# Optimization experiments

Hardware: AMD Instinct MI355X
Metric: run time of the kernel (lower is better)

Reference implementation:

```python
import jax, jax.numpy as jnp
import numpy as np

L = 6  # num_objects (greedy iterations)
BIG = 1e8  # penalty for already-used template ids (matches torch code)


def setup_inputs() -> dict:
    key = jax.random.key(0)
    k1, k2, k3, k4 = jax.random.split(key, 4)
    B, T, C, H, W = 16, 144, 1, 128, 128
    x = jax.random.uniform(k1, (B, C, H, W), jnp.float32)
    templates = jax.random.uniform(k2, (B, T, C, H, W), jnp.float32)
    masks = jax.random.uniform(k3, (B, T, 1, H, W), jnp.float32)
    background = jax.random.uniform(k4, (1, C, H, W), jnp.float32)
    return {"x": x, "templates": templates, "masks": masks, "background": background}


def _greedy_select(x, templates, masks, background):
    """Greedy template selection. Faithful to DecompModel._greedy_selection
    (use_empty is falsy by default -> empty template = 5*ones, empty mask = ones).
    Key identity used for efficiency: dead-leaves composition of the l
    already-selected objects is affine in whatever lies below them:
        recons = A + Mprod * below,
    where A accumulates painted objects and Mprod = prod(1 - mask_i).
    The new candidate at step l is painted BELOW the existing selection
    (it sits at the last index, and compose_templates paints last->first),
    so below = cand*cand_mask + bg*(1-cand_mask). Identical math, no
    O(B*T*l) recomposition per step."""
    B, T = templates.shape[0], templates.shape[1]
    H, W = templates.shape[-2], templates.shape[-1]
    empty_t = 5.0 * jnp.ones((B, 1) + templates.shape[2:], templates.dtype)
    empty_m = jnp.ones((B, 1) + masks.shape[2:], masks.dtype)
    temps = jnp.concatenate([empty_t, templates], axis=1)   # (B,T+1,C,H,W)
    ms = jnp.concatenate([empty_m, masks], axis=1)           # (B,T+1,1,H,W)
    bg = jnp.broadcast_to(background, (B,) + background.shape[1:])  # (B,C,H,W)

    A0 = jnp.zeros_like(bg)                                  # painted-so-far
    M0 = jnp.ones((B, 1, H, W), bg.dtype)                    # transmission
    used0 = jnp.zeros((B, T + 1), bool)
    bidx = jnp.arange(B)

    def step(carry, _):
        A, Mprod, used = carry
        below = temps * ms + bg[:, None] * (1.0 - ms)        # (B,T+1,C,H,W)
        recons = A[:, None] + Mprod[:, None] * below         # (B,T+1,C,H,W)
        errors = jnp.mean((x[:, None] - recons) ** 2, axis=(2, 3, 4))  # (B,T+1)
        errors = jnp.where(used, BIG, errors)
        ids = jnp.argmin(errors, axis=1)                     # (B,)
        hit = (jnp.arange(T + 1)[None, :] == ids[:, None]) & (ids[:, None] != 0)
        used = used | hit                                    # empty id=0 reusable
        sel_t = temps[bidx, ids]                             # (B,C,H,W)
        sel_m = ms[bidx, ids]                                # (B,1,H,W)
        A = A + Mprod * sel_t * sel_m
        Mprod = Mprod * (1.0 - sel_m)
        return (A, Mprod, used), ids

    (_, _, _), ids = jax.lax.scan(step, (A0, M0, used0), None, length=L)
    ids = ids.T                                              # (B,L)
    objects = temps[bidx[:, None], ids]                      # (B,L,C,H,W)
    omasks = ms[bidx[:, None], ids]                          # (B,L,1,H,W)
    return objects, omasks, ids


def _compose(objects, omasks, background):
    """Dead-leaves composition, painting from last object to first
    (first selected object ends up on top), as in compose_templates."""
    B, N = objects.shape[0], objects.shape[1]
    recons = jnp.broadcast_to(background, (B,) + background.shape[1:])
    for i in range(N):  # small fixed loop over L objects
        o = objects[:, N - 1 - i]
        m = omasks[:, N - 1 - i]
        recons = o * m + recons * (1.0 - m)
    return recons


def reference(x, templates, masks, background):
    objects, omasks, ids = _greedy_select(x, templates, masks, background)
    recons = _compose(objects, omasks, background)           # (B,C,H,W)
    return recons, objects, omasks, ids
```

## Files before the change

### kernel.cpp

```cpp
#include <hip/hip_runtime.h>
#include <math.h>

#define BB 16
#define TT 144
#define TP1 145
#define HW4 4096
#define HW8 2048
#define LL 6
#define BIGE 1e30
#define NB_STEP (BB * TP1)
#define CHUNK 290
#define EPSQ 7.62951e-6

typedef float          f4    __attribute__((ext_vector_type(4)));
typedef float          f8    __attribute__((ext_vector_type(8)));
typedef unsigned short u16x4 __attribute__((ext_vector_type(4)));
typedef unsigned short u16x8 __attribute__((ext_vector_type(8)));

static const size_t OFF_A     = 0;
static const size_t OFF_M     = 1u << 20;
static const size_t OFF_U     = 2u << 20;
static const size_t OFF_V     = 3u << 20;
static const size_t OFF_ERR32 = 4u << 20;
static const size_t OFF_ERR16 = (4u << 20) + 32768;
static const size_t OFF_D     = (4u << 20) + 65536;
static const size_t OFF_USED  = (4u << 20) + 81920;
static const size_t OFF_WQ    = (4u << 20) + 131072;
static const size_t WS_FULL   = OFF_WQ + 75497472ull;

__device__ __forceinline__ float hsum(f4 v) { return ((v.x + v.y) + v.z) + v.w; }
__device__ __forceinline__ float hsum8(f8 v) {
    return (((v.s0 + v.s1) + (v.s2 + v.s3)) + ((v.s4 + v.s5) + (v.s6 + v.s7)));
}

__device__ __forceinline__ double blk_reduce(double s) {
    for (int off = 32; off; off >>= 1) s += __shfl_down(s, off);
    __shared__ double smr[4];
    if ((threadIdx.x & 63) == 0) smr[threadIdx.x >> 6] = s;
    __syncthreads();
    return smr[0] + smr[1] + smr[2] + smr[3];
}

__device__ __forceinline__ void blk_reduce2(double& a, double& b) {
    for (int off = 32; off; off >>= 1) { a += __shfl_down(a, off); b += __shfl_down(b, off); }
    __shared__ double sa[4], sb[4];
    if ((threadIdx.x & 63) == 0) { sa[threadIdx.x >> 6] = a; sb[threadIdx.x >> 6] = b; }
    __syncthreads();
    a = sa[0] + sa[1] + sa[2] + sa[3];
    b = sb[0] + sb[1] + sb[2] + sb[3];
}

__global__ void k_build(const f4* __restrict__ temps, const f4* __restrict__ masks,
                        const f4* __restrict__ bg, const f4* __restrict__ x,
                        u16x4* __restrict__ wq, double* __restrict__ err32,
                        int* __restrict__ used) {
    const int t = blockIdx.x, b = blockIdx.y, tid = threadIdx.x;
    const f4* xb = x + (size_t)b * HW4;
    double s = 0.0;
    if (t == 0) {
        if (tid < TP1) used[b * TP1 + tid] = 0;
        for (int j = tid; j < HW4; j += 256)
            s += (double)(100.f - 10.f * hsum(xb[j]));
    } else {
        const size_t row = ((size_t)(b * TT + t - 1)) * HW4;
        for (int j = tid; j < HW4; j += 256) {
            f4 tv = __builtin_nontemporal_load(&temps[row + j]);
            f4 mv = __builtin_nontemporal_load(&masks[row + j]);
            f4 bv = bg[j], xv = xb[j];
            f4 w = tv * mv + bv * (1.f - mv);
            wq[row + j] = __builtin_convertvector(w * 65535.f + 0.5f, u16x4);
            s += (double)hsum(w * (w - 2.f * xv));
        }
    }
    double tot = blk_reduce(s);
    if (tid == 0) err32[b * TP1 + t] = tot;
}

__global__ void k_err16(const u16x8* __restrict__ wq,
                        const f4* __restrict__ u4, const f4* __restrict__ v4,
                        const int* __restrict__ used,
                        double* __restrict__ err16, double* __restrict__ D) {
    const int lin = blockIdx.x;
    const int wg  = (lin & 7) * CHUNK + (lin >> 3);
    const int b   = wg / TP1;
    const int t   = wg - b * TP1;
    const int tid = threadIdx.x;
    if (t != 0 && used[b * TP1 + t]) {
        if (tid == 0) err16[b * TP1 + t] = BIGE;
        return;
    }
    if (t == 0) {
        const f4* ub = u4 + (size_t)b * HW4;
        const f4* vb = v4 + (size_t)b * HW4;
        double s = 0.0, d = 0.0;
        for (int j = tid; j < HW4; j += 256) {
            f4 uu = ub[j], vv = vb[j];
            s += (double)(25.f * hsum(vv) - 10.f * hsum(uu));
            f4 au = {fabsf(uu.x), fabsf(uu.y), fabsf(uu.z), fabsf(uu.w)};
            d += (double)hsum(vv + au);
        }
        blk_reduce2(s, d);
        if (tid == 0) { err16[b * TP1] = s; D[b] = d; }
        return;
    }
    const f8* ub = (const f8*)(u4 + (size_t)b * HW4);
    const f8* vb = (const f8*)(v4 + (size_t)b * HW4);
    const u16x8* wb = wq + ((size_t)(b * TT + t - 1)) * HW8;
    double s = 0.0;
    for (int j = tid; j < HW8; j += 256) {
        f8 w = __builtin_convertvector(wb[j], f8) * (1.f / 65535.f);
        f8 uu = ub[j], vv = vb[j];
        s += (double)hsum8(w * (vv * w - 2.f * uu));
    }
    double tot = blk_reduce(s);
    if (tid == 0) err16[b * TP1 + t] = tot;
}

__global__ void k_refine(const f4* __restrict__ temps, const f4* __restrict__ masks,
                         const f4* __restrict__ bg,
                         const f4* __restrict__ u4, const f4* __restrict__ v4,
                         const double* __restrict__ err16, const double* __restrict__ D,
                         double* __restrict__ err32) {
    const int t = blockIdx.x, b = blockIdx.y, tid = threadIdx.x;
    double e = (tid < TP1) ? err16[b * TP1 + tid] : 1e300;
    double m = e;
    for (int off = 32; off; off >>= 1) {
        double o = __shfl_down(m, off);
        m = (o < m) ? o : m;
    }
    __shared__ double sm[4]; __shared__ double smin_s; __shared__ int scnt[4];
    if ((tid & 63) == 0) sm[tid >> 6] = m;
    __syncthreads();
    if (tid == 0) {
        double a = (sm[0] < sm[1]) ? sm[0] : sm[1];
        double c = (sm[2] < sm[3]) ? sm[2] : sm[3];
        smin_s = (a < c) ? a : c;
    }
    __syncthreads();
    const double thr = smin_s + (4.0 * EPSQ * D[b] + 0.05);
    int flag = (tid < TP1) && (e <= thr);
    unsigned long long bal = __ballot(flag);
    if ((tid & 63) == 0) scnt[tid >> 6] = __popcll(bal);
    __syncthreads();
    const int cnt = scnt[0] + scnt[1] + scnt[2] + scnt[3];
    const double mys = err16[b * TP1 + t];
    if (mys > thr) { if (tid == 0) err32[b * TP1 + t] = BIGE; return; }
    if (cnt == 1 || t == 0) {
        if (tid == 0) err32[b * TP1 + t] = mys;
        return;
    }
    const f4* ub = u4 + (size_t)b * HW4;
    const f4* vb = v4 + (size_t)b * HW4;
    const size_t row = ((size_t)(b * TT + t - 1)) * HW4;
    double s = 0.0;
    for (int j = tid; j < HW4; j += 256) {
        f4 tv = temps[row + j], mv = masks[row + j], bv = bg[j];
        f4 uu = ub[j], vv = vb[j];
        f4 w = tv * mv + bv * (1.f - mv);
        s += (double)hsum(w * (vv * w - 2.f * uu));
    }
    double tot = blk_reduce(s);
    if (tid == 0) err32[b * TP1 + t] = tot;
}

__global__ void k_err_f32(const f4* __restrict__ temps, const f4* __restrict__ masks,
                          const f4* __restrict__ bg,
                          const f4* __restrict__ u4, const f4* __restrict__ v4,
                          const int* __restrict__ used, double* __restrict__ err32) {
    const int t = blockIdx.x, b = blockIdx.y, tid = threadIdx.x;
    if (t != 0 && used[b * TP1 + t]) {
        if (tid == 0) err32[b * TP1 + t] = BIGE;
        return;
    }
    const f4* ub = u4 + (size_t)b * HW4;
    const f4* vb = v4 + (size_t)b * HW4;
    double s = 0.0;
    if (t == 0) {
        for (int j = tid; j < HW4; j += 256) {
            f4 uu = ub[j], vv = vb[j];
            s += (double)(25.f * hsum(vv) - 10.f * hsum(uu));
        }
    } else {
        const size_t row = ((size_t)(b * TT + t - 1)) * HW4;
        for (int j = tid; j < HW4; j += 256) {
            f4 tv = temps[row + j], mv = masks[row + j], bv = bg[j];
            f4 uu = ub[j], vv = vb[j];
            f4 w = tv * mv + bv * (1.f - mv);
            s += (double)hsum(w * (vv * w - 2.f * uu));
        }
    }
    double tot = blk_reduce(s);
    if (tid == 0) err32[b * TP1 + t] = tot;
}

template <bool FIRST, bool LAST>
__global__ void k_upd(const f4* __restrict__ temps, const f4* __restrict__ masks,
                      const f4* __restrict__ x, const f4* __restrict__ bg,
                      const double* __restrict__ err,
                      int* __restrict__ used, f4* __restrict__ A, f4* __restrict__ M,
                      f4* __restrict__ u, f4* __restrict__ v,
                      f4* __restrict__ out_obj, f4* __restrict__ out_msk,
                      f4* __restrict__ out_rec, float* __restrict__ out_ids, int l) {
    const int tid = threadIdx.x;
    const int gid = blockIdx.x * 256 + tid;
    const int b = gid >> 12;
    const int p = gid & (HW4 - 1);
    __shared__ int ssel;
    if (tid < 64) {
        double best = 1e301;
        int bi = TP1;
        for (int t = tid; t < TP1; t += 64) {
            double e = err[b * TP1 + t];
            if (e < best) { best = e; bi = t; }
        }
        for (int off = 32; off; off >>= 1) {
            double oe = __shfl_down(best, off);
            int    oi = __shfl_down(bi, off);
            if (oe < best || (oe == best && oi < bi)) { best = oe; bi = oi; }
        }
        if (tid == 0) ssel = bi;
    }
    __syncthreads();
    const int id = ssel;
    f4 st, sm;
    if (id == 0) {
        st = (f4){5.f, 5.f, 5.f, 5.f};
        sm = (f4){1.f, 1.f, 1.f, 1.f};
    } else {
        size_t base = ((size_t)(b * TT + id - 1)) * HW4 + p;
        st = temps[base];
        sm = masks[base];
    }
    f4 a, mp;
    if (FIRST) { a = (f4){0.f, 0.f, 0.f, 0.f}; mp = (f4){1.f, 1.f, 1.f, 1.f}; }
    else       { a = A[gid]; mp = M[gid]; }
    a = a + mp * st * sm;
    mp = mp * (1.f - sm);
    const size_t ob = ((size_t)(b * LL + l)) * HW4 + p;
    out_obj[ob] = st;
    out_msk[ob] = sm;
    if (LAST) {
        out_rec[gid] = a + mp * bg[p];
    } else {
        A[gid] = a; M[gid] = mp;
        f4 xv = x[gid];
        u[gid] = (xv - a) * mp;
        v[gid] = mp * mp;
    }
    if ((blockIdx.x & 15) == 0 && tid == 0) {
        if (id != 0) used[b * TP1 + id] = 1;
        out_ids[b * LL + l] = (float)id;
    }
}

__global__ void k_uv0(const f4* __restrict__ x, f4* __restrict__ u, f4* __restrict__ v,
                      int* __restrict__ used) {
    int gid = blockIdx.x * blockDim.x + threadIdx.x;
    if (gid < BB * TP1) used[gid] = 0;
    if (gid >= BB * HW4) return;
    u[gid] = x[gid];
    v[gid] = (f4){1.f, 1.f, 1.f, 1.f};
}

static inline void launch_upd(bool first, bool last,
                              const f4* temps, const f4* masks, const f4* x, const f4* bg,
                              const double* err, int* used, f4* A, f4* M,
                              f4* u, f4* v, f4* out_obj, f4* out_msk, f4* out_rec,
                              float* out_ids, int l, hipStream_t stream) {
    if (first)
        k_upd<true, false><<<256, 256, 0, stream>>>(temps, masks, x, bg, err, used, A, M, u, v, out_obj, out_msk, out_rec, out_ids, l);
    else if (last)
        k_upd<false, true><<<256, 256, 0, stream>>>(temps, masks, x, bg, err, used, A, M, u, v, out_obj, out_msk, out_rec, out_ids, l);
    else
        k_upd<false, false><<<256, 256, 0, stream>>>(temps, masks, x, bg, err, used, A, M, u, v, out_obj, out_msk, out_rec, out_ids, l);
}

extern "C" void kernel_launch(void* const* d_in, const int* in_sizes, int n_in,
                              void* d_out, int out_size, void* d_ws, size_t ws_size,
                              hipStream_t stream) {
    const f4* x     = (const f4*)d_in[0];
    const f4* temps = (const f4*)d_in[1];
    const f4* masks = (const f4*)d_in[2];
    const f4* bg    = (const f4*)d_in[3];

    float* out      = (float*)d_out;
    f4*    out_rec  = (f4*)out;
    f4*    out_obj  = (f4*)(out + 262144);
    f4*    out_msk  = (f4*)(out + 262144 + 1572864);
    float* out_ids  = out + 262144 + 2 * 1572864;

    char* ws = (char*)d_ws;
    f4*     A     = (f4*)(ws + OFF_A);
    f4*     M     = (f4*)(ws + OFF_M);
    f4*     u     = (f4*)(ws + OFF_U);
    f4*     v     = (f4*)(ws + OFF_V);
    double* err32 = (double*)(ws + OFF_ERR32);
    double* err16 = (double*)(ws + OFF_ERR16);
    double* D     = (double*)(ws + OFF_D);
    int*    used  = (int*)(ws + OFF_USED);
    u16x4*  wq    = (u16x4*)(ws + OFF_WQ);

    const bool full = (ws_size >= WS_FULL);

    if (full) {
        k_build<<<dim3(TP1, BB), 256, 0, stream>>>(temps, masks, bg, x, wq, err32, used);
        for (int l = 0; l < LL; ++l) {
            launch_upd(l == 0, l == LL - 1, temps, masks, x, bg, err32, used, A, M, u, v,
                       out_obj, out_msk, out_rec, out_ids, l, stream);
            if (l < LL - 1) {
                k_err16<<<NB_STEP, 256, 0, stream>>>((const u16x8*)wq, u, v, used, err16, D);
                k_refine<<<dim3(TP1, BB), 256, 0, stream>>>(temps, masks, bg, u, v, err16, D, err32);
            }
        }
    } else {
        k_uv0<<<(BB * HW4 + 255) / 256, 256, 0, stream>>>(x, u, v, used);
        for (int l = 0; l < LL; ++l) {
            k_err_f32<<<dim3(TP1, BB), 256, 0, stream>>>(temps, masks, bg, u, v, used, err32);
            launch_upd(l == 0, l == LL - 1, temps, masks, x, bg, err32, used, A, M, u, v,
                       out_obj, out_msk, out_rec, out_ids, l, stream);
        }
    }
}
```

Baseline: 257.3 us.

## Batch four templates per block and reformulate error as residual squared norm

Build and per-step error kernels now process four templates per block, so the per-batch u/v (now scaled-mask and residual) vectors are loaded once and reused across four template rows. The state is cut from four arrays (A, M, u, v) to two (scaled transmission and residual), and the error becomes a direct squared-difference sum instead of an expanded quadratic. Block indices are swizzled across XCD-sized groups, and the refine threshold is widened to allow for the new formulation's quantization error. This trades fewer resident blocks and a looser refine filter, which may send more candidates to the fp32 path, for less redundant memory traffic.

```diff
diff --git a/kernel.cpp b/kernel.cpp
--- a/kernel.cpp
+++ b/kernel.cpp
@@ -8,29 +8,37 @@
 #define HW8 2048
 #define LL 6
 #define BIGE 1e30
-#define NB_STEP (BB * TP1)
-#define CHUNK 290
 #define EPSQ 7.62951e-6
+#define RB 37
+#define NBLK (BB * RB)
+#define BCHUNK 74
+#define RCHUNK 290
 
 typedef float          f4    __attribute__((ext_vector_type(4)));
 typedef float          f8    __attribute__((ext_vector_type(8)));
 typedef unsigned short u16x4 __attribute__((ext_vector_type(4)));
 typedef unsigned short u16x8 __attribute__((ext_vector_type(8)));
 
-static const size_t OFF_A     = 0;
-static const size_t OFF_M     = 1u << 20;
-static const size_t OFF_U     = 2u << 20;
-static const size_t OFF_V     = 3u << 20;
-static const size_t OFF_ERR32 = 4u << 20;
-static const size_t OFF_ERR16 = (4u << 20) + 32768;
-static const size_t OFF_D     = (4u << 20) + 65536;
-static const size_t OFF_USED  = (4u << 20) + 81920;
-static const size_t OFF_WQ    = (4u << 20) + 131072;
-static const size_t WS_FULL   = OFF_WQ + 75497472ull;
+static const size_t OFF_MS   = 0;
+static const size_t OFF_R    = 1u << 20;
+static const size_t OFF_E32  = 2u << 20;
+static const size_t OFF_E16  = (2u << 20) + 32768;
+static const size_t OFF_D    = (2u << 20) + 65536;
+static const size_t OFF_USED = (2u << 20) + 81920;
+static const size_t OFF_WQ   = 3u << 20;
+static const size_t WS_FULL  = OFF_WQ + 75497472ull;
 
 __device__ __forceinline__ float hsum(f4 v) { return ((v.x + v.y) + v.z) + v.w; }
 __device__ __forceinline__ float hsum8(f8 v) {
     return (((v.s0 + v.s1) + (v.s2 + v.s3)) + ((v.s4 + v.s5) + (v.s6 + v.s7)));
+}
+__device__ __forceinline__ f8 fabs8(f8 v) {
+    f8 o;
+    o.s0 = __builtin_fabsf(v.s0); o.s1 = __builtin_fabsf(v.s1);
+    o.s2 = __builtin_fabsf(v.s2); o.s3 = __builtin_fabsf(v.s3);
+    o.s4 = __builtin_fabsf(v.s4); o.s5 = __builtin_fabsf(v.s5);
+    o.s6 = __builtin_fabsf(v.s6); o.s7 = __builtin_fabsf(v.s7);
+    return o;
 }
 
 __device__ __forceinline__ double blk_reduce(double s) {
@@ -50,78 +58,129 @@
     b = sb[0] + sb[1] + sb[2] + sb[3];
 }
 
+__device__ __forceinline__ void blk_reduce4(double s[4]) {
+    for (int off = 32; off; off >>= 1) {
+        s[0] += __shfl_down(s[0], off); s[1] += __shfl_down(s[1], off);
+        s[2] += __shfl_down(s[2], off); s[3] += __shfl_down(s[3], off);
+    }
+    __shared__ double sm4[4][4];
+    const int wv = threadIdx.x >> 6;
+    if ((threadIdx.x & 63) == 0) {
+        sm4[wv][0] = s[0]; sm4[wv][1] = s[1]; sm4[wv][2] = s[2]; sm4[wv][3] = s[3];
+    }
+    __syncthreads();
+    for (int k = 0; k < 4; ++k) s[k] = sm4[0][k] + sm4[1][k] + sm4[2][k] + sm4[3][k];
+}
+
 __global__ void k_build(const f4* __restrict__ temps, const f4* __restrict__ masks,
                         const f4* __restrict__ bg, const f4* __restrict__ x,
                         u16x4* __restrict__ wq, double* __restrict__ err32,
                         int* __restrict__ used) {
-    const int t = blockIdx.x, b = blockIdx.y, tid = threadIdx.x;
+    const int lin = blockIdx.x;
+    const int wg = (lin & 7) * BCHUNK + (lin >> 3);
+    const int b = wg / RB, rg = wg - b * RB;
+    const int tid = threadIdx.x;
     const f4* xb = x + (size_t)b * HW4;
-    double s = 0.0;
-    if (t == 0) {
+    if (rg == RB - 1) {
         if (tid < TP1) used[b * TP1 + tid] = 0;
-        for (int j = tid; j < HW4; j += 256)
-            s += (double)(100.f - 10.f * hsum(xb[j]));
-    } else {
-        const size_t row = ((size_t)(b * TT + t - 1)) * HW4;
+        double s = 0.0;
         for (int j = tid; j < HW4; j += 256) {
-            f4 tv = __builtin_nontemporal_load(&temps[row + j]);
-            f4 mv = __builtin_nontemporal_load(&masks[row + j]);
-            f4 bv = bg[j], xv = xb[j];
-            f4 w = tv * mv + bv * (1.f - mv);
-            wq[row + j] = __builtin_convertvector(w * 65535.f + 0.5f, u16x4);
-            s += (double)hsum(w * (w - 2.f * xv));
-        }
-    }
-    double tot = blk_reduce(s);
-    if (tid == 0) err32[b * TP1 + t] = tot;
-}
-
-__global__ void k_err16(const u16x8* __restrict__ wq,
-                        const f4* __restrict__ u4, const f4* __restrict__ v4,
-                        const int* __restrict__ used,
-                        double* __restrict__ err16, double* __restrict__ D) {
-    const int lin = blockIdx.x;
-    const int wg  = (lin & 7) * CHUNK + (lin >> 3);
-    const int b   = wg / TP1;
-    const int t   = wg - b * TP1;
-    const int tid = threadIdx.x;
-    if (t != 0 && used[b * TP1 + t]) {
-        if (tid == 0) err16[b * TP1 + t] = BIGE;
+            f4 d = 5.f - xb[j];
+            s += (double)hsum(d * d);
+        }
+        double tot = blk_reduce(s);
+        if (tid == 0) err32[b * TP1 + 0] = tot;
         return;
     }
-    if (t == 0) {
-        const f4* ub = u4 + (size_t)b * HW4;
-        const f4* vb = v4 + (size_t)b * HW4;
+    const int tbase = 1 + rg * 4;
+    const size_t r0 = ((size_t)(b * TT + tbase - 1)) * HW4;
+    const size_t r1 = r0 + HW4, r2 = r1 + HW4, r3 = r2 + HW4;
+    double s[4] = {0.0, 0.0, 0.0, 0.0};
+    #pragma unroll 2
+    for (int j = tid; j < HW4; j += 256) {
+        f4 bv = bg[j], xv = xb[j];
+        f4 tv0 = __builtin_nontemporal_load(&temps[r0 + j]);
+        f4 mv0 = __builtin_nontemporal_load(&masks[r0 + j]);
+        f4 w0 = tv0 * mv0 + bv * (1.f - mv0);
+        wq[r0 + j] = __builtin_convertvector(w0 * 65535.f + 0.5f, u16x4);
+        f4 d0 = w0 - xv; s[0] += (double)hsum(d0 * d0);
+        f4 tv1 = __builtin_nontemporal_load(&temps[r1 + j]);
+        f4 mv1 = __builtin_nontemporal_load(&masks[r1 + j]);
+        f4 w1 = tv1 * mv1 + bv * (1.f - mv1);
+        wq[r1 + j] = __builtin_convertvector(w1 * 65535.f + 0.5f, u16x4);
+        f4 d1 = w1 - xv; s[1] += (double)hsum(d1 * d1);
+        f4 tv2 = __builtin_nontemporal_load(&temps[r2 + j]);
+        f4 mv2 = __builtin_nontemporal_load(&masks[r2 + j]);
+        f4 w2 = tv2 * mv2 + bv * (1.f - mv2);
+        wq[r2 + j] = __builtin_convertvector(w2 * 65535.f + 0.5f, u16x4);
+        f4 d2 = w2 - xv; s[2] += (double)hsum(d2 * d2);
+        f4 tv3 = __builtin_nontemporal_load(&temps[r3 + j]);
+        f4 mv3 = __builtin_nontemporal_load(&masks[r3 + j]);
+        f4 w3 = tv3 * mv3 + bv * (1.f - mv3);
+        wq[r3 + j] = __builtin_convertvector(w3 * 65535.f + 0.5f, u16x4);
+        f4 d3 = w3 - xv; s[3] += (double)hsum(d3 * d3);
+    }
+    blk_reduce4(s);
+    if (tid == 0)
+        for (int k = 0; k < 4; ++k) err32[b * TP1 + tbase + k] = s[k];
+}
+
+__global__ void k_errs(const u16x8* __restrict__ wq,
+                       const f8* __restrict__ Ms, const f8* __restrict__ R,
+                       const int* __restrict__ used,
+                       double* __restrict__ err16, double* __restrict__ Dd) {
+    const int lin = blockIdx.x;
+    const int wg = (lin & 7) * BCHUNK + (lin >> 3);
+    const int b = wg / RB, rg = wg - b * RB;
+    const int tid = threadIdx.x;
+    const f8* msb = Ms + (size_t)b * HW8;
+    const f8* rb  = R  + (size_t)b * HW8;
+    if (rg == RB - 1) {
         double s = 0.0, d = 0.0;
-        for (int j = tid; j < HW4; j += 256) {
-            f4 uu = ub[j], vv = vb[j];
-            s += (double)(25.f * hsum(vv) - 10.f * hsum(uu));
-            f4 au = {fabsf(uu.x), fabsf(uu.y), fabsf(uu.z), fabsf(uu.w)};
-            d += (double)hsum(vv + au);
+        for (int j = tid; j < HW8; j += 256) {
+            f8 ms = msb[j], rr = rb[j];
+            f8 M = ms * 65535.f;
+            f8 dd = M * 5.f - rr;
+            s += (double)hsum8(dd * dd);
+            d += (double)hsum8(M * (M + fabs8(rr)));
         }
         blk_reduce2(s, d);
-        if (tid == 0) { err16[b * TP1] = s; D[b] = d; }
+        if (tid == 0) { err16[b * TP1 + 0] = s; Dd[b] = d; }
         return;
     }
-    const f8* ub = (const f8*)(u4 + (size_t)b * HW4);
-    const f8* vb = (const f8*)(v4 + (size_t)b * HW4);
-    const u16x8* wb = wq + ((size_t)(b * TT + t - 1)) * HW8;
-    double s = 0.0;
+    const int tbase = 1 + rg * 4;
+    const size_t r0 = ((size_t)(b * TT + tbase - 1)) * HW8;
+    const size_t r1 = r0 + HW8, r2 = r1 + HW8, r3 = r2 + HW8;
+    double s[4] = {0.0, 0.0, 0.0, 0.0};
+    #pragma unroll 2
     for (int j = tid; j < HW8; j += 256) {
-        f8 w = __builtin_convertvector(wb[j], f8) * (1.f / 65535.f);
-        f8 uu = ub[j], vv = vb[j];
-        s += (double)hsum8(w * (vv * w - 2.f * uu));
-    }
-    double tot = blk_reduce(s);
-    if (tid == 0) err16[b * TP1 + t] = tot;
+        f8 ms = msb[j], rr = rb[j];
+        f8 q0 = __builtin_convertvector(wq[r0 + j], f8);
+        f8 d0 = q0 * ms - rr; s[0] += (double)hsum8(d0 * d0);
+        f8 q1 = __builtin_convertvector(wq[r1 + j], f8);
+        f8 d1 = q1 * ms - rr; s[1] += (double)hsum8(d1 * d1);
+        f8 q2 = __builtin_convertvector(wq[r2 + j], f8);
+        f8 d2 = q2 * ms - rr; s[2] += (double)hsum8(d2 * d2);
+        f8 q3 = __builtin_convertvector(wq[r3 + j], f8);
+        f8 d3 = q3 * ms - rr; s[3] += (double)hsum8(d3 * d3);
+    }
+    blk_reduce4(s);
+    if (tid == 0)
+        for (int k = 0; k < 4; ++k) {
+            int t = tbase + k;
+            err16[b * TP1 + t] = used[b * TP1 + t] ? BIGE : s[k];
+        }
 }
 
 __global__ void k_refine(const f4* __restrict__ temps, const f4* __restrict__ masks,
                          const f4* __restrict__ bg,
-                         const f4* __restrict__ u4, const f4* __restrict__ v4,
-                         const double* __restrict__ err16, const double* __restrict__ D,
+                         const f4* __restrict__ Ms4, const f4* __restrict__ R4,
+                         const double* __restrict__ err16, const double* __restrict__ Dd,
                          double* __restrict__ err32) {
-    const int t = blockIdx.x, b = blockIdx.y, tid = threadIdx.x;
+    const int lin = blockIdx.x;
+    const int wg = (lin & 7) * RCHUNK + (lin >> 3);
+    const int b = wg / TP1, t = wg - b * TP1;
+    const int tid = threadIdx.x;
     double e = (tid < TP1) ? err16[b * TP1 + tid] : 1e300;
     double m = e;
     for (int off = 32; off; off >>= 1) {
@@ -137,7 +196,7 @@
         smin_s = (a < c) ? a : c;
     }
     __syncthreads();
-    const double thr = smin_s + (4.0 * EPSQ * D[b] + 0.05);
+    const double thr = smin_s + (6.0 * EPSQ * Dd[b] + 0.15);
     int flag = (tid < TP1) && (e <= thr);
     unsigned long long bal = __ballot(flag);
     if ((tid & 63) == 0) scnt[tid >> 6] = __popcll(bal);
@@ -145,134 +204,121 @@
     const int cnt = scnt[0] + scnt[1] + scnt[2] + scnt[3];
     const double mys = err16[b * TP1 + t];
     if (mys > thr) { if (tid == 0) err32[b * TP1 + t] = BIGE; return; }
-    if (cnt == 1 || t == 0) {
-        if (tid == 0) err32[b * TP1 + t] = mys;
-        return;
-    }
-    const f4* ub = u4 + (size_t)b * HW4;
-    const f4* vb = v4 + (size_t)b * HW4;
+    if (cnt == 1 || t == 0) { if (tid == 0) err32[b * TP1 + t] = mys; return; }
     const size_t row = ((size_t)(b * TT + t - 1)) * HW4;
+    const f4* msb = Ms4 + (size_t)b * HW4;
+    const f4* rb  = R4  + (size_t)b * HW4;
     double s = 0.0;
     for (int j = tid; j < HW4; j += 256) {
         f4 tv = temps[row + j], mv = masks[row + j], bv = bg[j];
-        f4 uu = ub[j], vv = vb[j];
         f4 w = tv * mv + bv * (1.f - mv);
-        s += (double)hsum(w * (vv * w - 2.f * uu));
+        f4 M = msb[j] * 65535.f;
+        f4 d = w * M - rb[j];
+        s += (double)hsum(d * d);
     }
     double tot = blk_reduce(s);
     if (tid == 0) err32[b * TP1 + t] = tot;
 }
 
-__global__ void k_err_f32(const f4* __restrict__ temps, const f4* __restrict__ masks,
-                          const f4* __restrict__ bg,
-                          const f4* __restrict__ u4, const f4* __restrict__ v4,
-                          const int* __restrict__ used, double* __restrict__ err32) {
-    const int t = blockIdx.x, b = blockIdx.y, tid = threadIdx.x;
+template <bool FIRST, bool LAST>
+__global__ void k_upd(const f4* __restrict__ temps, const f4* __restrict__ masks,
+                      const f4* __restrict__ x, const f4* __restrict__ bg,
+                      const double* __restrict__ err,
+                      int* __restrict__ used, f4* __restrict__ Ms4, f4* __restrict__ R4,
+                      f4* __restrict__ out_obj, f4* __restrict__ out_msk,
+                      f4* __restrict__ out_rec, float* __restrict__ out_ids, int l) {
+    const int lin = blockIdx.x;
+    const int wg = (lin & 7) * 32 + (lin >> 3);
+    const int tid = threadIdx.x;
+    const int gid = wg * 256 + tid;
+    const int b = gid >> 12;
+    const int p = gid & (HW4 - 1);
+    __shared__ int ssel;
+    if (tid < 64) {
+        double best = 1e301; int bi = TP1;
+        for (int t = tid; t < TP1; t += 64) {
+            double e = err[b * TP1 + t];
+            if (e < best) { best = e; bi = t; }
+        }
+        for (int off = 32; off; off >>= 1) {
+            double oe = __shfl_down(best, off);
+            int    oi = __shfl_down(bi, off);
+            if (oe < best || (oe == best && oi < bi)) { best = oe; bi = oi; }
+        }
+        if (tid == 0) ssel = bi;
+    }
+    __syncthreads();
+    const int id = ssel;
+    f4 st, sm_;
+    if (id == 0) { st = (f4){5.f,5.f,5.f,5.f}; sm_ = (f4){1.f,1.f,1.f,1.f}; }
+    else {
+        size_t base = ((size_t)(b * TT + id - 1)) * HW4 + p;
+        st = temps[base]; sm_ = masks[base];
+    }
+    f4 xv = x[gid];
+    f4 a, mp;
+    if (FIRST) { a = (f4){0.f,0.f,0.f,0.f}; mp = (f4){1.f,1.f,1.f,1.f}; }
+    else       { mp = Ms4[gid] * 65535.f; a = xv - R4[gid]; }
+    a = a + mp * st * sm_;
+    mp = mp * (1.f - sm_);
+    const size_t ob = ((size_t)(b * LL + l)) * HW4 + p;
+    out_obj[ob] = st;
+    out_msk[ob] = sm_;
+    if (LAST) {
+        out_rec[gid] = a + mp * bg[p];
+    } else {
+        Ms4[gid] = mp * (1.f / 65535.f);
+        R4[gid]  = xv - a;
+    }
+    if ((wg & 15) == 0 && tid == 0) {
+        if (id != 0) used[b * TP1 + id] = 1;
+        out_ids[b * LL + l] = (float)id;
+    }
+}
+
+__global__ void k_init0(const f4* __restrict__ x, f4* __restrict__ Ms4, f4* __restrict__ R4,
+                        int* __restrict__ used) {
+    int gid = blockIdx.x * blockDim.x + threadIdx.x;
+    if (gid < BB * TP1) used[gid] = 0;
+    if (gid >= BB * HW4) return;
+    float msv = (float)(1.0 / 65535.0);
+    Ms4[gid] = (f4){msv, msv, msv, msv};
+    R4[gid] = x[gid];
+}
+
+__global__ void k_errfb(const f4* __restrict__ temps, const f4* __restrict__ masks,
+                        const f4* __restrict__ bg,
+                        const f4* __restrict__ Ms4, const f4* __restrict__ R4,
+                        const int* __restrict__ used, double* __restrict__ err32) {
+    const int lin = blockIdx.x;
+    const int wg = (lin & 7) * RCHUNK + (lin >> 3);
+    const int b = wg / TP1, t = wg - b * TP1;
+    const int tid = threadIdx.x;
     if (t != 0 && used[b * TP1 + t]) {
         if (tid == 0) err32[b * TP1 + t] = BIGE;
         return;
     }
-    const f4* ub = u4 + (size_t)b * HW4;
-    const f4* vb = v4 + (size_t)b * HW4;
+    const f4* msb = Ms4 + (size_t)b * HW4;
+    const f4* rb  = R4  + (size_t)b * HW4;
     double s = 0.0;
     if (t == 0) {
         for (int j = tid; j < HW4; j += 256) {
-            f4 uu = ub[j], vv = vb[j];
-            s += (double)(25.f * hsum(vv) - 10.f * hsum(uu));
+            f4 M = msb[j] * 65535.f;
+            f4 d = M * 5.f - rb[j];
+            s += (double)hsum(d * d);
         }
     } else {
         const size_t row = ((size_t)(b * TT + t - 1)) * HW4;
         for (int j = tid; j < HW4; j += 256) {
             f4 tv = temps[row + j], mv = masks[row + j], bv = bg[j];
-            f4 uu = ub[j], vv = vb[j];
             f4 w = tv * mv + bv * (1.f - mv);
-            s += (double)hsum(w * (vv * w - 2.f * uu));
+            f4 M = msb[j] * 65535.f;
+            f4 d = w * M - rb[j];
+            s += (double)hsum(d * d);
         }
     }
     double tot = blk_reduce(s);
     if (tid == 0) err32[b * TP1 + t] = tot;
-}
-
-template <bool FIRST, bool LAST>
-__global__ void k_upd(const f4* __restrict__ temps, const f4* __restrict__ masks,
-                      const f4* __restrict__ x, const f4* __restrict__ bg,
-                      const double* __restrict__ err,
-                      int* __restrict__ used, f4* __restrict__ A, f4* __restrict__ M,
-                      f4* __restrict__ u, f4* __restrict__ v,
-                      f4* __restrict__ out_obj, f4* __restrict__ out_msk,
-                      f4* __restrict__ out_rec, float* __restrict__ out_ids, int l) {
-    const int tid = threadIdx.x;
-    const int gid = blockIdx.x * 256 + tid;
-    const int b = gid >> 12;
-    const int p = gid & (HW4 - 1);
-    __shared__ int ssel;
-    if (tid < 64) {
-        double best = 1e301;
-        int bi = TP1;
-        for (int t = tid; t < TP1; t += 64) {
-            double e = err[b * TP1 + t];
-            if (e < best) { best = e; bi = t; }
-        }
-        for (int off = 32; off; off >>= 1) {
-            double oe = __shfl_down(best, off);
-            int    oi = __shfl_down(bi, off);
-            if (oe < best || (oe == best && oi < bi)) { best = oe; bi = oi; }
-        }
-        if (tid == 0) ssel = bi;
-    }
-    __syncthreads();
-    const int id = ssel;
-    f4 st, sm;
-    if (id == 0) {
-        st = (f4){5.f, 5.f, 5.f, 5.f};
-        sm = (f4){1.f, 1.f, 1.f, 1.f};
-    } else {
-        size_t base = ((size_t)(b * TT + id - 1)) * HW4 + p;
-        st = temps[base];
-        sm = masks[base];
-    }
-    f4 a, mp;
-    if (FIRST) { a = (f4){0.f, 0.f, 0.f, 0.f}; mp = (f4){1.f, 1.f, 1.f, 1.f}; }
-    else       { a = A[gid]; mp = M[gid]; }
-    a = a + mp * st * sm;
-    mp = mp * (1.f - sm);
-    const size_t ob = ((size_t)(b * LL + l)) * HW4 + p;
-    out_obj[ob] = st;
-    out_msk[ob] = sm;
-    if (LAST) {
-        out_rec[gid] = a + mp * bg[p];
-    } else {
-        A[gid] = a; M[gid] = mp;
-        f4 xv = x[gid];
-        u[gid] = (xv - a) * mp;
-        v[gid] = mp * mp;
-    }
-    if ((blockIdx.x & 15) == 0 && tid == 0) {
-        if (id != 0) used[b * TP1 + id] = 1;
-        out_ids[b * LL + l] = (float)id;
-    }
-}
-
-__global__ void k_uv0(const f4* __restrict__ x, f4* __restrict__ u, f4* __restrict__ v,
-                      int* __restrict__ used) {
-    int gid = blockIdx.x * blockDim.x + threadIdx.x;
-    if (gid < BB * TP1) used[gid] = 0;
-    if (gid >= BB * HW4) return;
-    u[gid] = x[gid];
-    v[gid] = (f4){1.f, 1.f, 1.f, 1.f};
-}
-
-static inline void launch_upd(bool first, bool last,
-                              const f4* temps, const f4* masks, const f4* x, const f4* bg,
-                              const double* err, int* used, f4* A, f4* M,
-                              f4* u, f4* v, f4* out_obj, f4* out_msk, f4* out_rec,
-                              float* out_ids, int l, hipStream_t stream) {
-    if (first)
-        k_upd<true, false><<<256, 256, 0, stream>>>(temps, masks, x, bg, err, used, A, M, u, v, out_obj, out_msk, out_rec, out_ids, l);
-    else if (last)
-        k_upd<false, true><<<256, 256, 0, stream>>>(temps, masks, x, bg, err, used, A, M, u, v, out_obj, out_msk, out_rec, out_ids, l);
-    else
-        k_upd<false, false><<<256, 256, 0, stream>>>(temps, masks, x, bg, err, used, A, M, u, v, out_obj, out_msk, out_rec, out_ids, l);
 }
 
 extern "C" void kernel_launch(void* const* d_in, const int* in_sizes, int n_in,
@@ -290,34 +336,44 @@
     float* out_ids  = out + 262144 + 2 * 1572864;
 
     char* ws = (char*)d_ws;
-    f4*     A     = (f4*)(ws + OFF_A);
-    f4*     M     = (f4*)(ws + OFF_M);
-    f4*     u     = (f4*)(ws + OFF_U);
-    f4*     v     = (f4*)(ws + OFF_V);
-    double* err32 = (double*)(ws + OFF_ERR32);
-    double* err16 = (double*)(ws + OFF_ERR16);
-    double* D     = (double*)(ws + OFF_D);
+    f4*     Ms4   = (f4*)(ws + OFF_MS);
+    f4*     R4    = (f4*)(ws + OFF_R);
+    double* err32 = (double*)(ws + OFF_E32);
+    double* err16 = (double*)(ws + OFF_E16);
+    double* Dd    = (double*)(ws + OFF_D);
     int*    used  = (int*)(ws + OFF_USED);
     u16x4*  wq    = (u16x4*)(ws + OFF_WQ);
 
     const bool full = (ws_size >= WS_FULL);
 
     if (full) {
-        k_build<<<dim3(TP1, BB), 256, 0, stream>>>(temps, masks, bg, x, wq, err32, used);
+        k_build<<<NBLK, 256, 0, stream>>>(temps, masks, bg, x, wq, err32, used);
+        k_upd<true, false><<<256, 256, 0, stream>>>(temps, masks, x, bg, err32, used,
+                                                    Ms4, R4, out_obj, out_msk, out_rec, out_ids, 0);
+        for (int l = 1; l < LL; ++l) {
+            k_errs<<<NBLK, 256, 0, stream>>>((const u16x8*)wq, (const f8*)Ms4, (const f8*)R4,
+                                             used, err16, Dd);
+            k_refine<<<BB * TP1, 256, 0, stream>>>(temps, masks, bg, Ms4, R4, err16, Dd, err32);
+            if (l < LL - 1)
+                k_upd<false, false><<<256, 256, 0, stream>>>(temps, masks, x, bg, err32, used,
+                                                             Ms4, R4, out_obj, out_msk, out_rec, out_ids, l);
+            else
+                k_upd<false, true><<<256, 256, 0, stream>>>(temps, masks, x, bg, err32, used,
+                                                            Ms4, R4, out_obj, out_msk, out_rec, out_ids, l);
+        }
+    } else {
+        k_init0<<<(BB * HW4 + 255) / 256, 256, 0, stream>>>(x, Ms4, R4, used);
         for (int l = 0; l < LL; ++l) {
-            launch_upd(l == 0, l == LL - 1, temps, masks, x, bg, err32, used, A, M, u, v,
-                       out_obj, out_msk, out_rec, out_ids, l, stream);
-            if (l < LL - 1) {
-                k_err16<<<NB_STEP, 256, 0, stream>>>((const u16x8*)wq, u, v, used, err16, D);
-                k_refine<<<dim3(TP1, BB), 256, 0, stream>>>(temps, masks, bg, u, v, err16, D, err32);
-            }
-        }
-    } else {
-        k_uv0<<<(BB * HW4 + 255) / 256, 256, 0, stream>>>(x, u, v, used);
-        for (int l = 0; l < LL; ++l) {
-            k_err_f32<<<dim3(TP1, BB), 256, 0, stream>>>(temps, masks, bg, u, v, used, err32);
-            launch_upd(l == 0, l == LL - 1, temps, masks, x, bg, err32, used, A, M, u, v,
-                       out_obj, out_msk, out_rec, out_ids, l, stream);
-        }
-    }
-}
+            k_errfb<<<BB * TP1, 256, 0, stream>>>(temps, masks, bg, Ms4, R4, used, err32);
+            if (l == 0)
+                k_upd<true, false><<<256, 256, 0, stream>>>(temps, masks, x, bg, err32, used,
+                                                            Ms4, R4, out_obj, out_msk, out_rec, out_ids, l);
+            else if (l == LL - 1)
+                k_upd<false, true><<<256, 256, 0, stream>>>(temps, masks, x, bg, err32, used,
+                                                            Ms4, R4, out_obj, out_msk, out_rec, out_ids, l);
+            else
+                k_upd<false, false><<<256, 256, 0, stream>>>(temps, masks, x, bg, err32, used,
+                                                             Ms4, R4, out_obj, out_msk, out_rec, out_ids, l);
+        }
+    }
+}
```

New measurement: 240.4 us, median of 2. 1.07x faster.
